# Kernel optimization log

Measured on AMD Instinct MI355X. Metric: run time of the kernel, lower is better.

Reference implementation:

```python
import jax, jax.numpy as jnp
import numpy as np
import math

HIDDEN = 1024
N_HEADS = 16
N_KV = 4
HEAD_DIM = HIDDEN // N_HEADS  # 64
B, S = 2, 2048
THETA = 100000.0


def _freqs_cos_sin(dim, end, theta):
    # yarn params: original_max_position_embeddings=2048 >= end, so no ramp scaling,
    # attention_factor=1.0 -> plain RoPE frequencies.
    inv = 1.0 / theta ** (np.arange(0, dim, 2)[: dim // 2] / dim)
    t = np.arange(end)
    f = np.outer(t, inv).astype(np.float32)  # (end, dim/2)
    cos = np.concatenate([np.cos(f), np.cos(f)], axis=-1)  # (end, dim)
    sin = np.concatenate([np.sin(f), np.sin(f)], axis=-1)
    return jnp.asarray(cos), jnp.asarray(sin)


def _rotate(x):
    # stack([-x[...,1::2], x[...,::2]], -1).reshape_as(x)
    return jnp.stack([-x[..., 1::2], x[..., ::2]], axis=-1).reshape(x.shape)


def setup_inputs() -> dict:
    key = jax.random.key(0)
    ks = jax.random.split(key, 9)
    s = 0.02
    return {
        "hidden_states": jax.random.normal(ks[0], (B, S, HIDDEN), jnp.float32),
        "attention_mask": jnp.ones((B, S), jnp.int32),
        "Wq": jax.random.normal(ks[1], (HIDDEN, HIDDEN), jnp.float32) * s,
        "bq": jnp.zeros((HIDDEN,), jnp.float32),
        "Wk": jax.random.normal(ks[2], (HIDDEN, N_KV * HEAD_DIM), jnp.float32) * s,
        "bk": jnp.zeros((N_KV * HEAD_DIM,), jnp.float32),
        "Wv": jax.random.normal(ks[3], (HIDDEN, N_KV * HEAD_DIM), jnp.float32) * s,
        "bv": jnp.zeros((N_KV * HEAD_DIM,), jnp.float32),
        "Wo": jax.random.normal(ks[4], (HIDDEN, HIDDEN), jnp.float32) * s,
        "bo": jnp.zeros((HIDDEN,), jnp.float32),
    }


def reference(hidden_states, attention_mask, Wq, bq, Wk, bk, Wv, bv, Wo, bo):
    b, s, _ = hidden_states.shape
    q = (hidden_states @ Wq + bq).reshape(b, s, N_HEADS, HEAD_DIM)
    k = (hidden_states @ Wk + bk).reshape(b, s, N_KV, HEAD_DIM)
    v = (hidden_states @ Wv + bv).reshape(b, s, N_KV, HEAD_DIM)

    cos, sin = _freqs_cos_sin(HEAD_DIM, s, THETA)
    cos = cos[:, None, :]  # (s,1,d) broadcasts over (b,s,h,d)
    sin = sin[:, None, :]
    q = q * cos + _rotate(q) * sin
    k = k * cos + _rotate(k) * sin

    # GQA: repeat_interleave kv heads -> jnp.repeat along head axis
    rep = N_HEADS // N_KV
    k = jnp.repeat(k, rep, axis=2)
    v = jnp.repeat(v, rep, axis=2)

    scores = jnp.einsum("bqhd,bkhd->bhqk", q, k) / math.sqrt(HEAD_DIM)
    neg = jnp.finfo(scores.dtype).min
    causal = jnp.triu(jnp.ones((s, s), bool), k=1)  # (q,kv)
    bias = jnp.where(causal, neg, 0.0).astype(scores.dtype)[None, None]
    key_mask = attention_mask.astype(bool)[:, None, None, :]  # (b,1,1,kv)
    bias = jnp.where(key_mask, bias, neg)
    probs = jax.nn.softmax(scores + bias, axis=-1)
    attn = jnp.einsum("bhqk,bkhd->bqhd", probs, v).reshape(b, s, HIDDEN)
    return attn @ Wo + bo
```

## Files before the change

kernel.cpp:

```cpp
#include <hip/hip_runtime.h>
#include <cstddef>
#include <cstdint>

#define B_   2
#define S_   2048
#define HID  1024
#define NH_  16
#define NKV_ 4
#define DH_  64
#define ROWS (B_ * S_)
#define NQKV 1536
#define QSCALE 0.18033688011112042f

typedef __bf16 bf16_t;
typedef _Float16 f16_t;
typedef bf16_t bf16x8 __attribute__((ext_vector_type(8)));
typedef bf16_t bf16x4 __attribute__((ext_vector_type(4)));
typedef f16_t  f16x8  __attribute__((ext_vector_type(8)));
typedef f16_t  f16x4  __attribute__((ext_vector_type(4)));
typedef float  f32x4  __attribute__((ext_vector_type(4)));

typedef __attribute__((address_space(1))) const uint32_t gu32_t;
typedef __attribute__((address_space(3))) uint32_t lu32_t;

__device__ __forceinline__ void gl_lds16(const void* g, void* l) {
  __builtin_amdgcn_global_load_lds((gu32_t*)g, (lu32_t*)l, 16, 0, 0);
}

__global__ void prep_all(const float* __restrict__ hs,
                         const float* __restrict__ Wq, const float* __restrict__ Wk,
                         const float* __restrict__ Wv, const float* __restrict__ Wo,
                         const float* __restrict__ bq, const float* __restrict__ bk,
                         const float* __restrict__ bv,
                         bf16_t* __restrict__ hsb,
                         bf16_t* __restrict__ Wt, bf16_t* __restrict__ Wot,
                         float* __restrict__ ball, float2* __restrict__ lut)
{
  const int bid = blockIdx.x;
  if (bid < 2048) {
    const int i = (bid * 256 + threadIdx.x) * 8;
    float4 a = *(const float4*)(hs + i);
    float4 b = *(const float4*)(hs + i + 4);
    bf16x8 o;
    o[0]=(bf16_t)a.x; o[1]=(bf16_t)a.y; o[2]=(bf16_t)a.z; o[3]=(bf16_t)a.w;
    o[4]=(bf16_t)b.x; o[5]=(bf16_t)b.y; o[6]=(bf16_t)b.z; o[7]=(bf16_t)b.w;
    *(bf16x8*)(hsb + i) = o;
    return;
  }
  if (bid >= 4614) {
    const int idx = (bid - 4614) * 256 + threadIdx.x;
    const int s = idx >> 5, j = idx & 31;
    const float L = 0.51905126482615037f;
    const float ang = (float)s * exp2f(-L * (float)j);
    lut[idx] = make_float2(cosf(ang), sinf(ang));
    return;
  }
  if (bid >= 4608) {
    int i = (bid - 4608) * 256 + threadIdx.x;
    if (i < NQKV) ball[i] = (i < 1024) ? bq[i] : ((i < 1280) ? bk[i-1024] : bv[i-1280]);
    return;
  }
  const int wb = bid - 2048;
  const float* src; bf16_t* dst; int N, n0, k0;
  if (wb < 1024)      { src = Wq; dst = Wt;            N = 1024; int t = wb;      n0=(t&31)*32; k0=(t>>5)*32; }
  else if (wb < 1280) { src = Wk; dst = Wt + 1024*HID; N = 256;  int t = wb-1024; n0=(t&7)*32;  k0=(t>>3)*32; }
  else if (wb < 1536) { src = Wv; dst = Wt + 1280*HID; N = 256;  int t = wb-1280; n0=(t&7)*32;  k0=(t>>3)*32; }
  else                { src = Wo; dst = Wot;           N = 1024; int t = wb-1536; n0=(t&31)*32; k0=(t>>5)*32; }
  __shared__ bf16_t T[32][33];
  const int tx = threadIdx.x & 31, ty = threadIdx.x >> 5;
#pragma unroll
  for (int i = 0; i < 4; ++i)
    T[ty + i*8][tx] = (bf16_t)src[(size_t)(k0 + ty + i*8) * N + n0 + tx];
  __syncthreads();
#pragma unroll
  for (int i = 0; i < 4; ++i)
    dst[(size_t)(n0 + ty + i*8) * HID + k0 + tx] = T[tx][ty + i*8];
}

__global__ __launch_bounds__(256, 3) void gemm_qkv(
    const bf16_t* __restrict__ A, const bf16_t* __restrict__ Bt,
    const float* __restrict__ bias, const float2* __restrict__ lut,
    bf16_t* __restrict__ C, bf16_t* __restrict__ Kimg, f16_t* __restrict__ Vimg)
{
  __shared__ bf16_t As[2][128 * 64];
  __shared__ bf16_t Bs[2][64 * 64];
  const int tid  = threadIdx.x;
  const int w    = tid >> 6;
  const int lane = tid & 63;
  const int m    = lane & 15;
  const int quad = lane >> 4;
  const int wm   = w >> 1, wn = w & 1;

  const int lin = blockIdx.y * 24 + blockIdx.x;
  const int swz = (lin & 7) * 96 + (lin >> 3);
  const int bx  = swz % 24;
  const int by  = swz / 24;
  const size_t bm = (size_t)by * 128;
  const size_t bn = (size_t)bx * 64;

  const int srow = w * 8 + (lane >> 3);
  const int scol = (lane & 7) * 8;
  const bf16_t* Ag = A  + (bm + srow) * HID + scol;
  const bf16_t* Bg = Bt + (bn + srow) * HID + scol;

  f32x4 acc[4][2];
#pragma unroll
  for (int i = 0; i < 4; ++i)
#pragma unroll
    for (int j = 0; j < 2; ++j) acc[i][j] = (f32x4){0.f, 0.f, 0.f, 0.f};

#pragma unroll
  for (int i = 0; i < 4; ++i)
    gl_lds16(Ag + (size_t)(i * 32) * HID, &As[0][(w * 8 + i * 32) * 64]);
#pragma unroll
  for (int i = 0; i < 2; ++i)
    gl_lds16(Bg + (size_t)(i * 32) * HID, &Bs[0][(w * 8 + i * 32) * 64]);

  int p = 0;
  for (int k0 = 0; k0 < HID; k0 += 64) {
    __syncthreads();
    if (k0 + 64 < HID) {
#pragma unroll
      for (int i = 0; i < 4; ++i)
        gl_lds16(Ag + (size_t)(i * 32) * HID + k0 + 64, &As[p^1][(w * 8 + i * 32) * 64]);
#pragma unroll
      for (int i = 0; i < 2; ++i)
        gl_lds16(Bg + (size_t)(i * 32) * HID + k0 + 64, &Bs[p^1][(w * 8 + i * 32) * 64]);
    }
#pragma unroll
    for (int ks = 0; ks < 2; ++ks) {
      bf16x8 af[4], bfr[2];
#pragma unroll
      for (int mt = 0; mt < 4; ++mt)
        af[mt] = *(const bf16x8*)&As[p][(wm * 64 + mt * 16 + m) * 64 + ks * 32 + quad * 8];
#pragma unroll
      for (int nt = 0; nt < 2; ++nt)
        bfr[nt] = *(const bf16x8*)&Bs[p][(wn * 32 + nt * 16 + m) * 64 + ks * 32 + quad * 8];
#pragma unroll
      for (int mt = 0; mt < 4; ++mt)
#pragma unroll
        for (int nt = 0; nt < 2; ++nt)
          acc[mt][nt] = __builtin_amdgcn_mfma_f32_16x16x32_bf16(bfr[nt], af[mt], acc[mt][nt], 0, 0, 0);
    }
    p ^= 1;
  }

  const int b   = by >> 4;
  const int rt  = by & 15;

  if (bx < 16) {
#pragma unroll
    for (int mt = 0; mt < 4; ++mt) {
      const size_t row = bm + wm * 64 + mt * 16 + m;
#pragma unroll
      for (int nt = 0; nt < 2; ++nt) {
        const size_t col = bn + wn * 32 + nt * 16 + quad * 4;
        float4 bb = *(const float4*)&bias[col];
        bf16x4 o;
        o[0] = (bf16_t)(acc[mt][nt][0] + bb.x);
        o[1] = (bf16_t)(acc[mt][nt][1] + bb.y);
        o[2] = (bf16_t)(acc[mt][nt][2] + bb.z);
        o[3] = (bf16_t)(acc[mt][nt][3] + bb.w);
        *(bf16x4*)&C[row * NQKV + col] = o;
      }
    }
  } else if (bx < 20) {
    const int kvh = bx - 16;
    const size_t img0 = ((size_t)(b * NKV_ + kvh) * 32 + rt * 2) * 4096;
#pragma unroll
    for (int mt = 0; mt < 4; ++mt) {
      const int row128 = wm * 64 + mt * 16 + m;
      const int srw    = rt * 128 + row128;
      const int key    = row128 & 63;
      const size_t img = img0 + (size_t)(row128 >> 6) * 4096;
#pragma unroll
      for (int nt = 0; nt < 2; ++nt) {
        const int d0 = wn * 32 + nt * 16 + quad * 4;
        const float4 bb = *(const float4*)&bias[1024 + kvh * DH_ + d0];
        const float v0 = acc[mt][nt][0] + bb.x;
        const float v1 = acc[mt][nt][1] + bb.y;
        const float v2 = acc[mt][nt][2] + bb.z;
        const float v3 = acc[mt][nt][3] + bb.w;
        const float2* lp = lut + srw * 32 + (d0 & 31);
        const float2 l0 = lp[0], l1 = lp[1], l2 = lp[2], l3 = lp[3];
        bf16x4 o;
        o[0] = (bf16_t)(v0 * l0.x - v1 * l0.y);
        o[1] = (bf16_t)(v1 * l1.x + v0 * l1.y);
        o[2] = (bf16_t)(v2 * l2.x - v3 * l2.y);
        o[3] = (bf16_t)(v3 * l3.x + v2 * l3.y);
        const int slot = (d0 >> 3) ^ (key & 7);
        *(bf16x4*)&Kimg[img + key * 64 + slot * 8 + (d0 & 7)] = o;
      }
    }
  } else {
    const int kvh = bx - 20;
    f16_t* Lv = (f16_t*)&As[0][0];
    __syncthreads();
#pragma unroll
    for (int mt = 0; mt < 4; ++mt) {
      const int row128 = wm * 64 + mt * 16 + m;
#pragma unroll
      for (int nt = 0; nt < 2; ++nt) {
        const int d0 = wn * 32 + nt * 16 + quad * 4;
        const float4 bb = *(const float4*)&bias[1280 + kvh * DH_ + d0];
        f16x4 o;
        o[0] = (f16_t)(acc[mt][nt][0] + bb.x);
        o[1] = (f16_t)(acc[mt][nt][1] + bb.y);
        o[2] = (f16_t)(acc[mt][nt][2] + bb.z);
        o[3] = (f16_t)(acc[mt][nt][3] + bb.w);
        *(f16x4*)&Lv[row128 * 68 + d0] = o;
      }
    }
    __syncthreads();
    const size_t img0 = ((size_t)(b * NKV_ + kvh) * 32 + rt * 2) * 4096;
    const int d  = tid & 63;
    const int qg = tid >> 6;
#pragma unroll
    for (int i = 0; i < 8; ++i) {
      const int ki = i >> 2;
      const int g4 = qg * 4 + (i & 3);
      f16x4 o;
#pragma unroll
      for (int j = 0; j < 4; ++j)
        o[j] = Lv[(ki * 64 + g4 * 4 + j) * 68 + d];
      const int slot = g4 ^ (d & 15);
      *(f16x4*)&Vimg[img0 + (size_t)ki * 4096 + d * 64 + slot * 4] = o;
    }
  }
}

__global__ __launch_bounds__(256, 3) void gemm64_f32o(
    const bf16_t* __restrict__ A, const bf16_t* __restrict__ Bt,
    const float* __restrict__ bias, float* __restrict__ C, int N)
{
  __shared__ bf16_t As[2][128 * 64];
  __shared__ bf16_t Bs[2][64 * 64];
  const int tid  = threadIdx.x;
  const int w    = tid >> 6;
  const int lane = tid & 63;
  const int m    = lane & 15;
  const int quad = lane >> 4;
  const int wm   = w >> 1, wn = w & 1;

  const int lin = blockIdx.y * 16 + blockIdx.x;
  const int swz = (lin & 7) * 64 + (lin >> 3);
  const int bx  = swz & 15;
  const int by  = swz >> 4;
  const size_t bm = (size_t)by * 128;
  const size_t bn = (size_t)bx * 64;

  const int srow = w * 8 + (lane >> 3);
  const int scol = (lane & 7) * 8;
  const bf16_t* Ag = A  + (bm + srow) * HID + scol;
  const bf16_t* Bg = Bt + (bn + srow) * HID + scol;

  f32x4 acc[4][2];
#pragma unroll
  for (int i = 0; i < 4; ++i)
#pragma unroll
    for (int j = 0; j < 2; ++j) acc[i][j] = (f32x4){0.f, 0.f, 0.f, 0.f};

#pragma unroll
  for (int i = 0; i < 4; ++i)
    gl_lds16(Ag + (size_t)(i * 32) * HID, &As[0][(w * 8 + i * 32) * 64]);
#pragma unroll
  for (int i = 0; i < 2; ++i)
    gl_lds16(Bg + (size_t)(i * 32) * HID, &Bs[0][(w * 8 + i * 32) * 64]);

  int p = 0;
  for (int k0 = 0; k0 < HID; k0 += 64) {
    __syncthreads();
    if (k0 + 64 < HID) {
#pragma unroll
      for (int i = 0; i < 4; ++i)
        gl_lds16(Ag + (size_t)(i * 32) * HID + k0 + 64, &As[p^1][(w * 8 + i * 32) * 64]);
#pragma unroll
      for (int i = 0; i < 2; ++i)
        gl_lds16(Bg + (size_t)(i * 32) * HID + k0 + 64, &Bs[p^1][(w * 8 + i * 32) * 64]);
    }
#pragma unroll
    for (int ks = 0; ks < 2; ++ks) {
      bf16x8 af[4], bfr[2];
#pragma unroll
      for (int mt = 0; mt < 4; ++mt)
        af[mt] = *(const bf16x8*)&As[p][(wm * 64 + mt * 16 + m) * 64 + ks * 32 + quad * 8];
#pragma unroll
      for (int nt = 0; nt < 2; ++nt)
        bfr[nt] = *(const bf16x8*)&Bs[p][(wn * 32 + nt * 16 + m) * 64 + ks * 32 + quad * 8];
#pragma unroll
      for (int mt = 0; mt < 4; ++mt)
#pragma unroll
        for (int nt = 0; nt < 2; ++nt)
          acc[mt][nt] = __builtin_amdgcn_mfma_f32_16x16x32_bf16(bfr[nt], af[mt], acc[mt][nt], 0, 0, 0);
    }
    p ^= 1;
  }
#pragma unroll
  for (int mt = 0; mt < 4; ++mt) {
    const size_t row = bm + wm * 64 + mt * 16 + m;
#pragma unroll
    for (int nt = 0; nt < 2; ++nt) {
      const size_t col = bn + wn * 32 + nt * 16 + quad * 4;
      float4 bb = *(const float4*)&bias[col];
      float4 o;
      o.x = acc[mt][nt][0] + bb.x; o.y = acc[mt][nt][1] + bb.y;
      o.z = acc[mt][nt][2] + bb.z; o.w = acc[mt][nt][3] + bb.w;
      *(float4*)&C[row * N + col] = o;
    }
  }
}

#define PROC_TILE(AQ, OACC, LP, Q0W)                                          \
  do {                                                                        \
    f32x4 sc[4];                                                              \
    _Pragma("unroll") for (int cb = 0; cb < 4; ++cb)                          \
      sc[cb] = (f32x4){0.f, 0.f, 0.f, 0.f};                                   \
    _Pragma("unroll") for (int cb = 0; cb < 4; ++cb) {                        \
      const bf16x8 bk0 = *(const bf16x8*)&Ks[g][p][(cb*16 + m) * 64 + x0s * 8]; \
      const bf16x8 bk1 = *(const bf16x8*)&Ks[g][p][(cb*16 + m) * 64 + x1s * 8]; \
      sc[cb] = __builtin_amdgcn_mfma_f32_16x16x32_bf16(bk0, AQ[0], sc[cb], 0, 0, 0); \
      sc[cb] = __builtin_amdgcn_mfma_f32_16x16x32_bf16(bk1, AQ[1], sc[cb], 0, 0, 0); \
    }                                                                         \
    f16x4 bp[4];                                                              \
    {                                                                         \
      const bool needm = (kbase + 63 > (Q0W)) || (mb != ~0ull);               \
      if (needm) {                                                            \
        const int qv = (Q0W) + m;                                             \
        _Pragma("unroll") for (int cb = 0; cb < 4; ++cb)                      \
          _Pragma("unroll") for (int r = 0; r < 4; ++r) {                     \
            const int idx = cb*16 + quad*4 + r;                               \
            const bool ok = (kbase + idx <= qv) && ((mb >> idx) & 1);         \
            sc[cb][r] = ok ? sc[cb][r] : -1e38f;                              \
          }                                                                   \
      }                                                                       \
      float sum = 0.f;                                                        \
      _Pragma("unroll") for (int cb = 0; cb < 4; ++cb) {                      \
        f16x4 pp;                                                             \
        _Pragma("unroll") for (int r = 0; r < 4; ++r) {                       \
          const float pv = __builtin_amdgcn_exp2f(sc[cb][r]);                 \
          sum += pv;                                                          \
          pp[r] = (f16_t)pv;                                                  \
        }                                                                     \
        bp[cb] = pp;                                                          \
      }                                                                       \
      LP += sum;                                                              \
    }                                                                         \
    _Pragma("unroll") for (int cb = 0; cb < 4; ++cb) {                        \
      f16x4 av[4];                                                            \
      _Pragma("unroll") for (int dblk = 0; dblk < 4; ++dblk) {                \
        const int slot = (cb * 4 + quad) ^ m;                                 \
        av[dblk] = *(const f16x4*)&Vs[g][p][(dblk*16 + m) * 64 + slot * 4];   \
      }                                                                       \
      _Pragma("unroll") for (int dblk = 0; dblk < 4; ++dblk)                  \
        OACC[dblk] = __builtin_amdgcn_mfma_f32_16x16x16f16(av[dblk], bp[cb], OACC[dblk], 0, 0, 0); \
    }                                                                         \
  } while (0)

__global__ __launch_bounds__(512, 4) void attn_v11(
    const bf16_t* __restrict__ QKVb, const float2* __restrict__ lut,
    const bf16_t* __restrict__ Kt2, const f16_t* __restrict__ Vt2,
    const int* __restrict__ amask, bf16_t* __restrict__ Ab)
{
  __shared__ __align__(16) bf16_t Ks[2][2][64 * 64];
  __shared__ __align__(16) f16_t  Vs[2][2][64 * 64];

  const int tid  = threadIdx.x;
  const int w    = tid >> 6;
  const int g    = w >> 2;
  const int wl   = w & 3;
  const int lane = tid & 63;
  const int m    = lane & 15;
  const int quad = lane >> 4;
  const int kvh  = blockIdx.y;
  const int b    = blockIdx.z;
  const int h    = kvh * 4 + wl;
  const int x    = blockIdx.x;
  const int q0wA = x * 16;
  const int q0wB = (127 - x) * 16;
  const int nA   = (x >> 2) + 1;
  const int nB   = ((127 - x) >> 2) + 1;
  const int T    = nA + nB;

  bf16x8 aqA[2], aqB[2];
#pragma unroll
  for (int tt = 0; tt < 2; ++tt) {
    const int q0w_t = tt ? q0wB : q0wA;
    const int spos = q0w_t + m;
    const bf16_t* qsrc = QKVb + (size_t)(b * S_ + spos) * NQKV + h * DH_;
    float2 l8[8];
#pragma unroll
    for (int j = 0; j < 8; ++j) l8[j] = lut[spos * 32 + quad * 8 + j];
#pragma unroll
    for (int kc = 0; kc < 2; ++kc) {
      bf16x8 xv = *(const bf16x8*)(qsrc + kc * 32 + quad * 8);
      bf16x8 y;
#pragma unroll
      for (int i = 0; i < 4; ++i) {
        const float x0 = (float)xv[2*i], x1 = (float)xv[2*i+1];
        y[2*i]   = (bf16_t)((x0 * l8[2*i].x   - x1 * l8[2*i].y)   * QSCALE);
        y[2*i+1] = (bf16_t)((x1 * l8[2*i+1].x + x0 * l8[2*i+1].y) * QSCALE);
      }
      if (tt) aqB[kc] = y; else aqA[kc] = y;
    }
  }

  f32x4 oaccA[4], oaccB[4];
#pragma unroll
  for (int d = 0; d < 4; ++d) {
    oaccA[d] = (f32x4){0.f,0.f,0.f,0.f};
    oaccB[d] = (f32x4){0.f,0.f,0.f,0.f};
  }
  float lpA = 0.f, lpB = 0.f;

  const size_t imgbase = ((size_t)(b * NKV_ + kvh) * 32) * 4096;
  const bf16_t* Kg = Kt2 + imgbase;
  const f16_t*  Vg = Vt2 + imgbase;
  const int x0s = quad ^ (m & 7);
  const int x1s = (4 + quad) ^ (m & 7);
  const int* amp = amask + b * S_;

  int mcur;
  {
    const int e0  = g;
    const int kt0 = (e0 >= nA) ? e0 - nA : e0;
    const size_t off = (size_t)kt0 * 4096;
    gl_lds16(Kg + off + (2*wl)   * 512 + lane * 8, &Ks[g][0][(2*wl)   * 512]);
    gl_lds16(Kg + off + (2*wl+1) * 512 + lane * 8, &Ks[g][0][(2*wl+1) * 512]);
    gl_lds16(Vg + off + (2*wl)   * 512 + lane * 8, &Vs[g][0][(2*wl)   * 512]);
    gl_lds16(Vg + off + (2*wl+1) * 512 + lane * 8, &Vs[g][0][(2*wl+1) * 512]);
    mcur = amp[kt0 * 64 + lane];
  }

  int p = 0;
  const int niter = (T + 1) >> 1;
  for (int t = 0; t < niter; ++t) {
    const int e = 2 * t + g;
    __syncthreads();
    const int e2 = e + 2;
    const bool more = (e2 < T);
    int kt2 = 0;
    if (more) {
      kt2 = (e2 >= nA) ? e2 - nA : e2;
      const size_t off = (size_t)kt2 * 4096;
      gl_lds16(Kg + off + (2*wl)   * 512 + lane * 8, &Ks[g][p^1][(2*wl)   * 512]);
      gl_lds16(Kg + off + (2*wl+1) * 512 + lane * 8, &Ks[g][p^1][(2*wl+1) * 512]);
      gl_lds16(Vg + off + (2*wl)   * 512 + lane * 8, &Vs[g][p^1][(2*wl)   * 512]);
      gl_lds16(Vg + off + (2*wl+1) * 512 + lane * 8, &Vs[g][p^1][(2*wl+1) * 512]);
    }
    const int mnext = more ? amp[kt2 * 64 + lane] : 0;
    if (e < T) {
      const uint64_t mb = __ballot(mcur != 0);
      const bool isB = (e >= nA);
      const int kt = isB ? e - nA : e;
      const int kbase = kt * 64;
      if (isB) PROC_TILE(aqB, oaccB, lpB, q0wB);
      else     PROC_TILE(aqA, oaccA, lpA, q0wA);
    }
    mcur = mnext;
    p ^= 1;
  }

  float lAred = lpA;
  lAred += __shfl_xor(lAred, 16); lAred += __shfl_xor(lAred, 32);
  float lBred = lpB;
  lBred += __shfl_xor(lBred, 16); lBred += __shfl_xor(lBred, 32);

  __syncthreads();
  float* scrA = (float*)&Ks[0][0][0];
  float* scrB = (float*)&Vs[0][0][0];
  const int sbase = wl * 1104 + m * 68 + quad * 4;

  if (g == 0) {
#pragma unroll
    for (int dblk = 0; dblk < 4; ++dblk)
      *(f32x4*)&scrA[sbase + dblk * 16] = oaccA[dblk];
    if (quad == 0) scrA[wl * 1104 + 16 * 68 + m] = lAred;
  } else {
#pragma unroll
    for (int dblk = 0; dblk < 4; ++dblk)
      *(f32x4*)&scrB[sbase + dblk * 16] = oaccB[dblk];
    if (quad == 0) scrB[wl * 1104 + 16 * 68 + m] = lBred;
  }
  __syncthreads();

  if (g == 0) {
    const float l = lBred + scrB[wl * 1104 + 16 * 68 + m];
    const float inv = 1.0f / l;
    const size_t row = (size_t)(b * S_ + q0wB + m);
#pragma unroll
    for (int dblk = 0; dblk < 4; ++dblk) {
      const f32x4 part = *(const f32x4*)&scrB[sbase + dblk * 16];
      bf16x4 o;
      o[0] = (bf16_t)((oaccB[dblk][0] + part[0]) * inv);
      o[1] = (bf16_t)((oaccB[dblk][1] + part[1]) * inv);
      o[2] = (bf16_t)((oaccB[dblk][2] + part[2]) * inv);
      o[3] = (bf16_t)((oaccB[dblk][3] + part[3]) * inv);
      *(bf16x4*)&Ab[row * HID + h * DH_ + dblk * 16 + quad * 4] = o;
    }
  } else {
    const float l = lAred + scrA[wl * 1104 + 16 * 68 + m];
    const float inv = 1.0f / l;
    const size_t row = (size_t)(b * S_ + q0wA + m);
#pragma unroll
    for (int dblk = 0; dblk < 4; ++dblk) {
      const f32x4 part = *(const f32x4*)&scrA[sbase + dblk * 16];
      bf16x4 o;
      o[0] = (bf16_t)((oaccA[dblk][0] + part[0]) * inv);
      o[1] = (bf16_t)((oaccA[dblk][1] + part[1]) * inv);
      o[2] = (bf16_t)((oaccA[dblk][2] + part[2]) * inv);
      o[3] = (bf16_t)((oaccA[dblk][3] + part[3]) * inv);
      *(bf16x4*)&Ab[row * HID + h * DH_ + dblk * 16 + quad * 4] = o;
    }
  }
}

extern "C" void kernel_launch(void* const* d_in, const int* in_sizes, int n_in,
                              void* d_out, int out_size, void* d_ws, size_t ws_size,
                              hipStream_t stream)
{
  const float* hs    = (const float*)d_in[0];
  const int*   amask = (const int*)  d_in[1];
  const float* Wq    = (const float*)d_in[2];
  const float* bq    = (const float*)d_in[3];
  const float* Wk    = (const float*)d_in[4];
  const float* bk    = (const float*)d_in[5];
  const float* Wv    = (const float*)d_in[6];
  const float* bv    = (const float*)d_in[7];
  const float* Wo    = (const float*)d_in[8];
  const float* bo    = (const float*)d_in[9];
  float* out = (float*)d_out;

  bf16_t* QKVb = (bf16_t*)d_ws;
  bf16_t* hsb  = QKVb + (size_t)ROWS * NQKV;
  bf16_t* Wt   = hsb + (size_t)ROWS * HID;
  bf16_t* Wot  = Wt + (size_t)NQKV * HID;
  float*  ball = (float*)(Wot + (size_t)HID * HID);
  bf16_t* Kimg = (bf16_t*)(ball + NQKV);
  f16_t*  Vimg = (f16_t*)(Kimg + (size_t)B_*NKV_*32*4096);
  float2* lut  = (float2*)(Vimg + (size_t)B_*NKV_*32*4096);
  bf16_t* Ab   = hsb;

  prep_all<<<4870, 256, 0, stream>>>(hs, Wq, Wk, Wv, Wo, bq, bk, bv,
                                     hsb, Wt, Wot, ball, lut);

  gemm_qkv<<<dim3(NQKV/64, ROWS/128), 256, 0, stream>>>(hsb, Wt, ball, lut,
                                                        QKVb, Kimg, Vimg);

  attn_v11<<<dim3(64, NKV_, B_), 512, 0, stream>>>(QKVb, lut, Kimg, Vimg, amask, Ab);

  gemm64_f32o<<<dim3(HID/64, ROWS/128), 256, 0, stream>>>(Ab, Wot, bo, out, HID);
}
```

Measured before the change: 173.5 us.

## Split attention KV into 32-row tiles across four wave groups per block

The attention kernel now uses 1024 threads, with four wave groups each handling a different 32-key tile instead of two groups on 64-key tiles. The V image layout written by the QKV GEMM changes to 32-wide swizzled tiles to match. Partial accumulators from the groups are reduced through shared memory in two passes (A then B). The intent is more parallelism per block to cover the causal workload, at the cost of extra syncs, a larger reduction, and 64KB of LDS per block, which limits residency.

```diff
diff --git a/kernel.cpp b/kernel.cpp
--- a/kernel.cpp
+++ b/kernel.cpp
@@ -212,19 +212,19 @@
       }
     }
     __syncthreads();
-    const size_t img0 = ((size_t)(b * NKV_ + kvh) * 32 + rt * 2) * 4096;
+    const size_t imgb = ((size_t)(b * NKV_ + kvh) * 64 + rt * 4) * 2048;
     const int d  = tid & 63;
     const int qg = tid >> 6;
 #pragma unroll
     for (int i = 0; i < 8; ++i) {
-      const int ki = i >> 2;
-      const int g4 = qg * 4 + (i & 3);
+      const int ki = i >> 1;
+      const int g8 = qg * 2 + (i & 1);
       f16x4 o;
 #pragma unroll
       for (int j = 0; j < 4; ++j)
-        o[j] = Lv[(ki * 64 + g4 * 4 + j) * 68 + d];
-      const int slot = g4 ^ (d & 15);
-      *(f16x4*)&Vimg[img0 + (size_t)ki * 4096 + d * 64 + slot * 4] = o;
+        o[j] = Lv[(ki * 32 + g8 * 4 + j) * 68 + d];
+      const int slot = g8 ^ (d & 7);
+      *(f16x4*)&Vimg[imgb + (size_t)ki * 2048 + d * 32 + slot * 4] = o;
     }
   }
 }
@@ -310,23 +310,24 @@
   }
 }
 
-#define PROC_TILE(AQ, OACC, LP, Q0W)                                          \
+#define PROC_T32(AQ, OACC, LP, Q0W)                                           \
   do {                                                                        \
-    f32x4 sc[4];                                                              \
-    _Pragma("unroll") for (int cb = 0; cb < 4; ++cb)                          \
-      sc[cb] = (f32x4){0.f, 0.f, 0.f, 0.f};                                   \
-    _Pragma("unroll") for (int cb = 0; cb < 4; ++cb) {                        \
-      const bf16x8 bk0 = *(const bf16x8*)&Ks[g][p][(cb*16 + m) * 64 + x0s * 8]; \
-      const bf16x8 bk1 = *(const bf16x8*)&Ks[g][p][(cb*16 + m) * 64 + x1s * 8]; \
+    const bf16_t* kp = Ksb + (g * 2 + p) * 2048;                              \
+    const f16_t*  vp = Vsb + (g * 2 + p) * 2048;                              \
+    f32x4 sc[2];                                                              \
+    sc[0] = (f32x4){0.f,0.f,0.f,0.f}; sc[1] = (f32x4){0.f,0.f,0.f,0.f};       \
+    _Pragma("unroll") for (int cb = 0; cb < 2; ++cb) {                        \
+      const bf16x8 bk0 = *(const bf16x8*)(kp + (cb*16 + m) * 64 + x0s * 8);   \
+      const bf16x8 bk1 = *(const bf16x8*)(kp + (cb*16 + m) * 64 + x1s * 8);   \
       sc[cb] = __builtin_amdgcn_mfma_f32_16x16x32_bf16(bk0, AQ[0], sc[cb], 0, 0, 0); \
       sc[cb] = __builtin_amdgcn_mfma_f32_16x16x32_bf16(bk1, AQ[1], sc[cb], 0, 0, 0); \
     }                                                                         \
-    f16x4 bp[4];                                                              \
+    f16x4 bp[2];                                                              \
     {                                                                         \
-      const bool needm = (kbase + 63 > (Q0W)) || (mb != ~0ull);               \
+      const bool needm = (kbase + 31 > (Q0W)) || (mb != ~0ull);               \
       if (needm) {                                                            \
         const int qv = (Q0W) + m;                                             \
-        _Pragma("unroll") for (int cb = 0; cb < 4; ++cb)                      \
+        _Pragma("unroll") for (int cb = 0; cb < 2; ++cb)                      \
           _Pragma("unroll") for (int r = 0; r < 4; ++r) {                     \
             const int idx = cb*16 + quad*4 + r;                               \
             const bool ok = (kbase + idx <= qv) && ((mb >> idx) & 1);         \
@@ -334,7 +335,7 @@
           }                                                                   \
       }                                                                       \
       float sum = 0.f;                                                        \
-      _Pragma("unroll") for (int cb = 0; cb < 4; ++cb) {                      \
+      _Pragma("unroll") for (int cb = 0; cb < 2; ++cb) {                      \
         f16x4 pp;                                                             \
         _Pragma("unroll") for (int r = 0; r < 4; ++r) {                       \
           const float pv = __builtin_amdgcn_exp2f(sc[cb][r]);                 \
@@ -345,24 +346,23 @@
       }                                                                       \
       LP += sum;                                                              \
     }                                                                         \
-    _Pragma("unroll") for (int cb = 0; cb < 4; ++cb) {                        \
-      f16x4 av[4];                                                            \
+    _Pragma("unroll") for (int cb = 0; cb < 2; ++cb) {                        \
+      const int slot = (cb * 4 + quad) ^ (m & 7);                             \
       _Pragma("unroll") for (int dblk = 0; dblk < 4; ++dblk) {                \
-        const int slot = (cb * 4 + quad) ^ m;                                 \
-        av[dblk] = *(const f16x4*)&Vs[g][p][(dblk*16 + m) * 64 + slot * 4];   \
+        const f16x4 av = *(const f16x4*)(vp + (dblk*16 + m) * 32 + slot * 4); \
+        OACC[dblk] = __builtin_amdgcn_mfma_f32_16x16x16f16(av, bp[cb], OACC[dblk], 0, 0, 0); \
       }                                                                       \
-      _Pragma("unroll") for (int dblk = 0; dblk < 4; ++dblk)                  \
-        OACC[dblk] = __builtin_amdgcn_mfma_f32_16x16x16f16(av[dblk], bp[cb], OACC[dblk], 0, 0, 0); \
     }                                                                         \
   } while (0)
 
-__global__ __launch_bounds__(512, 4) void attn_v11(
+__global__ __launch_bounds__(1024, 8) void attn_v12(
     const bf16_t* __restrict__ QKVb, const float2* __restrict__ lut,
     const bf16_t* __restrict__ Kt2, const f16_t* __restrict__ Vt2,
     const int* __restrict__ amask, bf16_t* __restrict__ Ab)
 {
-  __shared__ __align__(16) bf16_t Ks[2][2][64 * 64];
-  __shared__ __align__(16) f16_t  Vs[2][2][64 * 64];
+  __shared__ __align__(16) uint8_t SMEM[65536];
+  bf16_t* Ksb = (bf16_t*)SMEM;
+  f16_t*  Vsb = (f16_t*)(SMEM + 32768);
 
   const int tid  = threadIdx.x;
   const int w    = tid >> 6;
@@ -377,9 +377,7 @@
   const int x    = blockIdx.x;
   const int q0wA = x * 16;
   const int q0wB = (127 - x) * 16;
-  const int nA   = (x >> 2) + 1;
-  const int nB   = ((127 - x) >> 2) + 1;
-  const int T    = nA + nB;
+  const int nA   = (x >> 1) + 1;
 
   bf16x8 aqA[2], aqB[2];
 #pragma unroll
@@ -412,7 +410,7 @@
   }
   float lpA = 0.f, lpB = 0.f;
 
-  const size_t imgbase = ((size_t)(b * NKV_ + kvh) * 32) * 4096;
+  const size_t imgbase = (size_t)(b * NKV_ + kvh) * 131072;
   const bf16_t* Kg = Kt2 + imgbase;
   const f16_t*  Vg = Vt2 + imgbase;
   const int x0s = quad ^ (m & 7);
@@ -423,92 +421,97 @@
   {
     const int e0  = g;
     const int kt0 = (e0 >= nA) ? e0 - nA : e0;
-    const size_t off = (size_t)kt0 * 4096;
-    gl_lds16(Kg + off + (2*wl)   * 512 + lane * 8, &Ks[g][0][(2*wl)   * 512]);
-    gl_lds16(Kg + off + (2*wl+1) * 512 + lane * 8, &Ks[g][0][(2*wl+1) * 512]);
-    gl_lds16(Vg + off + (2*wl)   * 512 + lane * 8, &Vs[g][0][(2*wl)   * 512]);
-    gl_lds16(Vg + off + (2*wl+1) * 512 + lane * 8, &Vs[g][0][(2*wl+1) * 512]);
-    mcur = amp[kt0 * 64 + lane];
+    gl_lds16(Kg + (size_t)kt0 * 2048 + wl * 512 + lane * 8, Ksb + (g*2) * 2048 + wl * 512);
+    gl_lds16(Vg + (size_t)kt0 * 2048 + wl * 512 + lane * 8, Vsb + (g*2) * 2048 + wl * 512);
+    mcur = amp[kt0 * 32 + (lane & 31)];
   }
 
   int p = 0;
-  const int niter = (T + 1) >> 1;
-  for (int t = 0; t < niter; ++t) {
-    const int e = 2 * t + g;
+  for (int t = 0; t < 17; ++t) {
+    const int e = 4 * t + g;
     __syncthreads();
-    const int e2 = e + 2;
-    const bool more = (e2 < T);
-    int kt2 = 0;
+    const int e4 = e + 4;
+    const bool more = (e4 < 65);
+    int ktn = 0;
     if (more) {
-      kt2 = (e2 >= nA) ? e2 - nA : e2;
-      const size_t off = (size_t)kt2 * 4096;
-      gl_lds16(Kg + off + (2*wl)   * 512 + lane * 8, &Ks[g][p^1][(2*wl)   * 512]);
-      gl_lds16(Kg + off + (2*wl+1) * 512 + lane * 8, &Ks[g][p^1][(2*wl+1) * 512]);
-      gl_lds16(Vg + off + (2*wl)   * 512 + lane * 8, &Vs[g][p^1][(2*wl)   * 512]);
-      gl_lds16(Vg + off + (2*wl+1) * 512 + lane * 8, &Vs[g][p^1][(2*wl+1) * 512]);
-    }
-    const int mnext = more ? amp[kt2 * 64 + lane] : 0;
-    if (e < T) {
+      ktn = (e4 >= nA) ? e4 - nA : e4;
+      gl_lds16(Kg + (size_t)ktn * 2048 + wl * 512 + lane * 8, Ksb + (g*2 + (p^1)) * 2048 + wl * 512);
+      gl_lds16(Vg + (size_t)ktn * 2048 + wl * 512 + lane * 8, Vsb + (g*2 + (p^1)) * 2048 + wl * 512);
+    }
+    const int mnext = more ? amp[ktn * 32 + (lane & 31)] : 0;
+    if (e < 65) {
       const uint64_t mb = __ballot(mcur != 0);
       const bool isB = (e >= nA);
       const int kt = isB ? e - nA : e;
-      const int kbase = kt * 64;
-      if (isB) PROC_TILE(aqB, oaccB, lpB, q0wB);
-      else     PROC_TILE(aqA, oaccA, lpA, q0wA);
+      const int kbase = kt * 32;
+      if (isB) PROC_T32(aqB, oaccB, lpB, q0wB);
+      else     PROC_T32(aqA, oaccA, lpA, q0wA);
     }
     mcur = mnext;
     p ^= 1;
   }
 
-  float lAred = lpA;
-  lAred += __shfl_xor(lAred, 16); lAred += __shfl_xor(lAred, 32);
-  float lBred = lpB;
-  lBred += __shfl_xor(lBred, 16); lBred += __shfl_xor(lBred, 32);
+  float lA = lpA; lA += __shfl_xor(lA, 16); lA += __shfl_xor(lA, 32);
+  float lB = lpB; lB += __shfl_xor(lB, 16); lB += __shfl_xor(lB, 32);
+
+  float* scr = (float*)SMEM;
+  const int sb_ = m * 68 + quad * 4;
 
   __syncthreads();
-  float* scrA = (float*)&Ks[0][0][0];
-  float* scrB = (float*)&Vs[0][0][0];
-  const int sbase = wl * 1104 + m * 68 + quad * 4;
-
+  if (g >= 1) {
+    float* r = scr + (g - 1) * 4416 + wl * 1104;
+#pragma unroll
+    for (int dblk = 0; dblk < 4; ++dblk)
+      *(f32x4*)&r[sb_ + dblk * 16] = oaccA[dblk];
+    if (quad == 0) r[1088 + m] = lA;
+  }
+  __syncthreads();
   if (g == 0) {
+    float l = lA;
+#pragma unroll
+    for (int rg = 0; rg < 3; ++rg) l += scr[rg * 4416 + wl * 1104 + 1088 + m];
+    const float inv = 1.0f / l;
+    const size_t row = (size_t)(b * S_ + q0wA + m);
+#pragma unroll
+    for (int dblk = 0; dblk < 4; ++dblk) {
+      f32x4 s = oaccA[dblk];
+#pragma unroll
+      for (int rg = 0; rg < 3; ++rg)
+        s += *(const f32x4*)&scr[rg * 4416 + wl * 1104 + sb_ + dblk * 16];
+      bf16x4 o;
+      o[0] = (bf16_t)(s[0] * inv);
+      o[1] = (bf16_t)(s[1] * inv);
+      o[2] = (bf16_t)(s[2] * inv);
+      o[3] = (bf16_t)(s[3] * inv);
+      *(bf16x4*)&Ab[row * HID + h * DH_ + dblk * 16 + quad * 4] = o;
+    }
+  }
+  __syncthreads();
+  if (g >= 1) {
+    float* r = scr + (g - 1) * 4416 + wl * 1104;
 #pragma unroll
     for (int dblk = 0; dblk < 4; ++dblk)
-      *(f32x4*)&scrA[sbase + dblk * 16] = oaccA[dblk];
-    if (quad == 0) scrA[wl * 1104 + 16 * 68 + m] = lAred;
-  } else {
-#pragma unroll
-    for (int dblk = 0; dblk < 4; ++dblk)
-      *(f32x4*)&scrB[sbase + dblk * 16] = oaccB[dblk];
-    if (quad == 0) scrB[wl * 1104 + 16 * 68 + m] = lBred;
+      *(f32x4*)&r[sb_ + dblk * 16] = oaccB[dblk];
+    if (quad == 0) r[1088 + m] = lB;
   }
   __syncthreads();
-
   if (g == 0) {
-    const float l = lBred + scrB[wl * 1104 + 16 * 68 + m];
+    float l = lB;
+#pragma unroll
+    for (int rg = 0; rg < 3; ++rg) l += scr[rg * 4416 + wl * 1104 + 1088 + m];
     const float inv = 1.0f / l;
     const size_t row = (size_t)(b * S_ + q0wB + m);
 #pragma unroll
     for (int dblk = 0; dblk < 4; ++dblk) {
-      const f32x4 part = *(const f32x4*)&scrB[sbase + dblk * 16];
+      f32x4 s = oaccB[dblk];
+#pragma unroll
+      for (int rg = 0; rg < 3; ++rg)
+        s += *(const f32x4*)&scr[rg * 4416 + wl * 1104 + sb_ + dblk * 16];
       bf16x4 o;
-      o[0] = (bf16_t)((oaccB[dblk][0] + part[0]) * inv);
-      o[1] = (bf16_t)((oaccB[dblk][1] + part[1]) * inv);
-      o[2] = (bf16_t)((oaccB[dblk][2] + part[2]) * inv);
-      o[3] = (bf16_t)((oaccB[dblk][3] + part[3]) * inv);
-      *(bf16x4*)&Ab[row * HID + h * DH_ + dblk * 16 + quad * 4] = o;
-    }
-  } else {
-    const float l = lAred + scrA[wl * 1104 + 16 * 68 + m];
-    const float inv = 1.0f / l;
-    const size_t row = (size_t)(b * S_ + q0wA + m);
-#pragma unroll
-    for (int dblk = 0; dblk < 4; ++dblk) {
-      const f32x4 part = *(const f32x4*)&scrA[sbase + dblk * 16];
-      bf16x4 o;
-      o[0] = (bf16_t)((oaccA[dblk][0] + part[0]) * inv);
-      o[1] = (bf16_t)((oaccA[dblk][1] + part[1]) * inv);
-      o[2] = (bf16_t)((oaccA[dblk][2] + part[2]) * inv);
-      o[3] = (bf16_t)((oaccA[dblk][3] + part[3]) * inv);
+      o[0] = (bf16_t)(s[0] * inv);
+      o[1] = (bf16_t)(s[1] * inv);
+      o[2] = (bf16_t)(s[2] * inv);
+      o[3] = (bf16_t)(s[3] * inv);
       *(bf16x4*)&Ab[row * HID + h * DH_ + dblk * 16 + quad * 4] = o;
     }
   }
@@ -546,7 +549,7 @@
   gemm_qkv<<<dim3(NQKV/64, ROWS/128), 256, 0, stream>>>(hsb, Wt, ball, lut,
                                                         QKVb, Kimg, Vimg);
 
-  attn_v11<<<dim3(64, NKV_, B_), 512, 0, stream>>>(QKVb, lut, Kimg, Vimg, amask, Ab);
+  attn_v12<<<dim3(64, NKV_, B_), 1024, 0, stream>>>(QKVb, lut, Kimg, Vimg, amask, Ab);
 
   gemm64_f32o<<<dim3(HID/64, ROWS/128), 256, 0, stream>>>(Ab, Wot, bo, out, HID);
 }
```

New measurement: 390.6 us. 2.25x slower.
